# Optimization experiments

Measured on AMD Instinct MI355X. Metric: run time of the kernel, lower is better.

## Reference

```python
import jax, jax.numpy as jnp
import numpy as np

D_MODEL = 192
NODE_NUM = 64
DEPTH = 2
ALPHA = 0.05
NUM_LAYERS = 2
LN_EPS = 1e-5


def _gcn(x, p):
    # x: [N, in_dim*D_MODEL]; faithful port of GCN.forward (eval mode)
    nv1, nv2, ws, bs, wm, bm, we, be, wl, bl, g, b = p
    N = x.shape[0]
    in_dim = x.shape[1] // D_MODEL
    adp = jax.nn.softmax(jax.nn.relu(nv1 @ nv2), axis=1)            # [V,V]
    adj = adp + jnp.eye(NODE_NUM, dtype=x.dtype)
    a = adj / adj.sum(1, keepdims=True)                              # row-normalized
    h0 = jax.lax.conv_general_dilated(
        x.reshape(N, in_dim, D_MODEL), ws, (1,), 'VALID',
        dimension_numbers=('NCH', 'OIH', 'NCH')) + bs[None, :, None]  # [N,C,V]
    h = h0
    outs = [h0]
    for _ in range(DEPTH):
        h = ALPHA * h0 + (1.0 - ALPHA) * jnp.einsum('ncw,vw->ncv', h, a)
        outs.append(h)
    ho = jnp.concatenate(outs, axis=1)                               # [N,(DEPTH+1)C,V]
    ho = jax.nn.gelu(jnp.einsum('ncv,oc->nov', ho, wm) + bm[None, :, None], approximate=False)
    ho = jnp.einsum('ncv,oc->nov', ho, we) + be[None, :, None]       # [N,6,V]
    ho = jnp.einsum('nov,dv->nod', ho, wl) + bl                      # [N,6,D]
    mu = ho.mean(-1, keepdims=True)
    var = ((ho - mu) ** 2).mean(-1, keepdims=True)                   # biased, like torch LN
    ho = (ho - mu) / jnp.sqrt(var + LN_EPS) * g + b
    return ho.reshape(N, 6 * D_MODEL)


def _encoder(inp4, flag, layer_params):
    x = jnp.transpose(inp4, (2, 0, 1, 3)) if flag == 1 else jnp.transpose(inp4, (1, 0, 2, 3))
    W, B, O, D = x.shape
    L = W + O - 1
    N = W * B
    # input_transfer: shift row r by r along the slice axis
    place = jax.vmap(lambda xr, r: jax.lax.dynamic_update_slice(
        jnp.zeros((B, L, D), x.dtype), xr, (0, r, 0)))
    a = place(x, jnp.arange(W)).reshape(N, L, D)
    layer0_output = None
    output_all = None
    rows_layers, cols_layers = [], []
    for layer in range(NUM_LAYERS):
        if layer >= 1:
            a = output_all  # eval mode: F.dropout is identity
            if layer == 1:
                layer0_output = a
        p = layer_params[layer]

        def step(carry, x_t, p=p):
            h_row, h_col = carry
            gate = _gcn(jnp.concatenate([h_row, h_col, x_t], axis=-1), p)  # [N,6D]
            sg = jax.nn.sigmoid(gate[:, :4 * D])
            tg = jnp.tanh(gate[:, 4 * D:])
            ug_r, og_r, ug_c, og_c = jnp.split(sg, 4, axis=-1)
            ig_r, ig_c = jnp.split(tg, 2, axis=-1)
            h_row = jnp.tanh((1.0 - ug_r) * h_row + ug_r * ig_r) * og_r
            h_col = jnp.tanh((1.0 - ug_c) * h_col + ug_c * ig_c) * og_c
            out_s = jnp.concatenate([h_row, h_col], axis=-1)
            # col hidden is saved pre-roll, rolled for next step
            return (h_row, jnp.roll(h_col, B, axis=0)), (out_s, h_row, h_col)

        init = (jnp.zeros((N, D), x.dtype), jnp.zeros((N, D), x.dtype))
        _, (outs, hrows, hcols) = jax.lax.scan(step, init, jnp.swapaxes(a, 0, 1))
        output_all = jnp.swapaxes(outs, 0, 1)                        # [N,L,2D]
        if layer >= 1:
            output_all = output_all + layer0_output
        # rows saved at slice s>=O-1 from block loc = s-O+1
        rows = hrows.reshape(L, W, B, D)[jnp.arange(O - 1, L), jnp.arange(W)]  # [W,B,D]
        # cols saved at slice s>=W-1 from last batch block
        cols = hcols[W - 1:, (W - 1) * B:, :]                        # [O,B,D]
        rows_layers.append(rows)
        cols_layers.append(cols)
    hidden_row_all = jnp.stack(rows_layers).transpose(2, 0, 1, 3)    # [B,layers,W,D]
    hidden_col_all = jnp.stack(cols_layers).transpose(2, 0, 1, 3)    # [B,layers,O,D]
    if flag == 1:
        return output_all, hidden_col_all, hidden_row_all
    return output_all, hidden_row_all, hidden_col_all


def setup_inputs() -> dict:
    key = jax.random.key(0)
    ks = jax.random.split(key, 20)
    idx = [0]
    def nxt():
        k = ks[idx[0]]
        idx[0] += 1
        return k
    B, W, O = 8, 24, 48
    K = D_MODEL - NODE_NUM + 1  # 129
    cc, sc, nd = 16, 32, 40
    d = {"input": jax.random.normal(nxt(), (B, W, O, D_MODEL), dtype=jnp.float32)}
    for li, in_dim in enumerate([3, 4]):
        d[f"nodevec1_{li}"] = jax.random.normal(nxt(), (NODE_NUM, nd), dtype=jnp.float32)
        d[f"nodevec2_{li}"] = jax.random.normal(nxt(), (nd, NODE_NUM), dtype=jnp.float32)
        d[f"w_start_{li}"] = jax.random.normal(nxt(), (cc, in_dim, K), dtype=jnp.float32) * 0.05
        d[f"b_start_{li}"] = jnp.zeros((cc,), jnp.float32)
        d[f"w_mlp_{li}"] = jax.random.normal(nxt(), (sc, (DEPTH + 1) * cc), dtype=jnp.float32) * 0.05
        d[f"b_mlp_{li}"] = jnp.zeros((sc,), jnp.float32)
        d[f"w_end_{li}"] = jax.random.normal(nxt(), (6, sc), dtype=jnp.float32) * 0.05
        d[f"b_end_{li}"] = jnp.zeros((6,), jnp.float32)
        d[f"w_lin_{li}"] = jax.random.normal(nxt(), (D_MODEL, NODE_NUM), dtype=jnp.float32) * 0.05
        d[f"b_lin_{li}"] = jnp.zeros((D_MODEL,), jnp.float32)
        d[f"gamma_{li}"] = jnp.ones((D_MODEL,), jnp.float32)
        d[f"beta_{li}"] = jnp.zeros((D_MODEL,), jnp.float32)
    d["flag"] = 0
    return d


def reference(input, nodevec1_0, nodevec2_0, w_start_0, b_start_0, w_mlp_0, b_mlp_0,
              w_end_0, b_end_0, w_lin_0, b_lin_0, gamma_0, beta_0,
              nodevec1_1, nodevec2_1, w_start_1, b_start_1, w_mlp_1, b_mlp_1,
              w_end_1, b_end_1, w_lin_1, b_lin_1, gamma_1, beta_1, flag):
    p0 = (nodevec1_0, nodevec2_0, w_start_0, b_start_0, w_mlp_0, b_mlp_0,
          w_end_0, b_end_0, w_lin_0, b_lin_0, gamma_0, beta_0)
    p1 = (nodevec1_1, nodevec2_1, w_start_1, b_start_1, w_mlp_1, b_mlp_1,
          w_end_1, b_end_1, w_lin_1, b_lin_1, gamma_1, beta_1)
    return _encoder(input, flag, (p0, p1))
```

## Files before the change

### kernel.cpp

```cpp
#include <hip/hip_runtime.h>
#include <hip/hip_bf16.h>

#define NT 256
typedef unsigned short u16;

__device__ __forceinline__ u16 tobf(float x) {
  union { __hip_bfloat16 h; u16 u; } cv;
  cv.h = __float2bfloat16(x);
  return cv.u;
}
__device__ __forceinline__ float frombf(u16 u) {
  return __uint_as_float(((unsigned)u) << 16);
}
__device__ __forceinline__ float sigf(float x) {
  return __builtin_amdgcn_rcpf(1.f + __builtin_amdgcn_exp2f(-1.4426950408889634f * x));
}
__device__ __forceinline__ float tanh_fast(float x) {
  return 1.f - 2.f * __builtin_amdgcn_rcpf(1.f + __builtin_amdgcn_exp2f(2.8853900817779268f * x));
}

struct SeqArgs {
  const float* input;
  const float* nv1_0; const float* nv2_0; const float* nv1_1; const float* nv2_1;
  const float* w_start0; const float* b_start0; const float* w_mlp0; const float* b_mlp0;
  const float* w_end0;   const float* b_end0;   const float* w_lin0; const float* b_lin0;
  const float* gamma0;   const float* beta0;
  const float* w_start1; const float* b_start1; const float* w_mlp1; const float* b_mlp1;
  const float* w_end1;   const float* b_end1;   const float* w_lin1; const float* b_lin1;
  const float* gamma1;   const float* beta1;
  float* HCOL;
  int*   flags;
  float* out_all; float* out_hrow; float* out_hcol;
};

__global__ __launch_bounds__(NT, 1) void seq_kernel(SeqArgs A) {
  const int n = blockIdx.x, w = n >> 3, b = n & 7, tid = threadIdx.x;
  const int pred = (n + 184) % 192;

  __shared__ __align__(16) float sCIN[768];
  __shared__ __align__(16) u16   sWS[64 * 132];
  __shared__ __align__(16) float sAT[4096];
  __shared__ __align__(16) float sH[2][1024];
  __shared__ __align__(16) float sAbuf[4928];
  float* const sPart = sAbuf;
  float* const sG    = sAbuf;
  float* const sE    = sAbuf + 2048;
  float* const sY    = sAbuf;
  float* const smWE  = sAbuf + 3072;
  float* const smBE  = sAbuf + 3264;
  float* const smWM  = sAbuf + 3328;

  for (int layer = 0; layer < 2; ++layer) {
    const int in_dim = 3 + layer;
    const int P = in_dim - 1;
    const float* nv1    = layer ? A.nv1_1    : A.nv1_0;
    const float* nv2    = layer ? A.nv2_1    : A.nv2_0;
    const float* wstart = layer ? A.w_start1 : A.w_start0;
    const float* bs     = layer ? A.b_start1 : A.b_start0;
    const float* wm     = layer ? A.w_mlp1   : A.w_mlp0;
    const float* bm     = layer ? A.b_mlp1   : A.b_mlp0;
    const float* we     = layer ? A.w_end1   : A.w_end0;
    const float* be     = layer ? A.b_end1   : A.b_end0;
    const float* wl     = layer ? A.w_lin1   : A.w_lin0;
    const float* bl     = layer ? A.b_lin1   : A.b_lin0;
    const float* gm     = layer ? A.gamma1   : A.gamma0;
    const float* bt     = layer ? A.beta1    : A.beta0;

    for (int idx = tid; idx < 4096; idx += NT) {
      int v = idx >> 6, ww = idx & 63;
      float s = 0.f;
      for (int j = 0; j < 40; ++j) s = fmaf(nv1[v*40 + j], nv2[j*64 + ww], s);
      sAbuf[idx] = fmaxf(s, 0.f);
    }
    __syncthreads();
    if (tid < 64) {
      const int v = tid;
      float m = -1e30f;
      for (int ww = 0; ww < 64; ++ww) m = fmaxf(m, sAbuf[v*64 + ww]);
      float s = 0.f;
      for (int ww = 0; ww < 64; ++ww) { float e = expf(sAbuf[v*64 + ww] - m); sAbuf[v*64 + ww] = e; s += e; }
      float inv = 1.f / s, rs = 1.f;
      for (int ww = 0; ww < 64; ++ww) rs += sAbuf[v*64 + ww] * inv;
      float irs = 1.f / rs;
      for (int ww = 0; ww < 64; ++ww) {
        float a = sAbuf[v*64 + ww] * inv + ((ww == v) ? 1.f : 0.f);
        sAT[ww*64 + v] = a * irs;
      }
    }
    __syncthreads();
    for (int idx = tid; idx < 16*in_dim*132; idx += NT) {
      int row = idx / 132, k = idx - row*132;
      sWS[idx] = (k < 129) ? tobf(wstart[((row & 15)*in_dim + (row >> 4))*129 + k]) : (u16)0;
    }
    for (int idx = tid; idx < 1536; idx += NT) { int o = idx/48, c = idx - o*48; smWM[o*50 + c] = wm[idx]; }
    for (int idx = tid; idx < 192; idx += NT) smWE[idx] = we[idx];
    if (tid < 6) smBE[tid] = be[tid];
    for (int d = tid; d < 384; d += NT) sCIN[d] = 0.f;

    const int o_m = tid >> 3, v8 = (tid & 7)*8;
    const int v_p = tid & 63, cq = tid >> 6;
    const float bmv = bm[o_m];
    float blv = 0.f, gmv = 1.f, btv = 0.f;
    if (tid < 192) { blv = bl[tid]; gmv = gm[tid]; btv = bt[tid]; }
    float bs_r[4];
#pragma unroll
    for (int m = 0; m < 4; ++m) bs_r[m] = bs[(tid >> 6) + 4*m];
    __syncthreads();

    auto pre_phase = [&](int t) {
      if (layer == 0) {
        int o = t - w;
        if (o >= 0 && o < 48) {
          const float* xr = A.input + (((size_t)(b*24 + w)*48 + o)*192);
          for (int d = tid; d < 192; d += NT) sCIN[384 + d] = xr[d];
        } else {
          for (int d = tid; d < 192; d += NT) sCIN[384 + d] = 0.f;
        }
      } else {
        const float* xr = A.out_all + ((size_t)n*71 + t)*384;
        for (int d = tid; d < 384; d += NT) sCIN[384 + d] = xr[d];
      }
      __syncthreads();
      {
        const int ci = tid >> 2, vq = tid & 3;
        const int p = ci >> 4, c = ci & 15;
        if (p < P) {
          const int ich = (p == 0) ? 0 : (p + 1);
          float acc[16];
#pragma unroll
          for (int j = 0; j < 16; ++j) acc[j] = 0.f;
          const float* xin = (p == 0) ? &sCIN[vq*16] : &sCIN[384 + (p-1)*192 + vq*16];
          const u16* wrow = &sWS[(ich*16 + c)*132];
          for (int k4 = 0; k4 < 128; k4 += 4) {
            ushort4 wu = *(const ushort4*)(wrow + k4);
            float w0 = frombf(wu.x), w1 = frombf(wu.y), w2 = frombf(wu.z), w3 = frombf(wu.w);
            union { float4 v4[5]; float f[20]; } X;
#pragma unroll
            for (int m = 0; m < 5; ++m) X.v4[m] = *(const float4*)(xin + k4 + 4*m);
#pragma unroll
            for (int j = 0; j < 16; ++j) {
              acc[j] = fmaf(w0, X.f[j],   acc[j]);
              acc[j] = fmaf(w1, X.f[j+1], acc[j]);
              acc[j] = fmaf(w2, X.f[j+2], acc[j]);
              acc[j] = fmaf(w3, X.f[j+3], acc[j]);
            }
          }
          {
            float wk = frombf(wrow[128]);
            union { float4 v4[4]; float f[16]; } X;
#pragma unroll
            for (int m = 0; m < 4; ++m) X.v4[m] = *(const float4*)(xin + 128 + 4*m);
#pragma unroll
            for (int j = 0; j < 16; ++j) acc[j] = fmaf(wk, X.f[j], acc[j]);
          }
          float* pp = &sPart[(p*16 + c)*64 + vq*16];
#pragma unroll
          for (int m = 0; m < 4; ++m)
            *(float4*)(pp + 4*m) = make_float4(acc[4*m], acc[4*m+1], acc[4*m+2], acc[4*m+3]);
        }
      }
      __syncthreads();
      {
        int m = 0;
        for (int idx = tid; idx < 1024; idx += NT, ++m) {
          int c = idx >> 6, v = idx & 63;
          float s = bs_r[m];
          for (int p = 0; p < P; ++p) s += sPart[(p*16 + c)*64 + v];
          sH[0][idx] = s;
        }
      }
      __syncthreads();
    };
    pre_phase(0);

    for (int t = 0; t < 71; ++t) {
      const int S = layer*71 + t;

      if (t > 0) {
        if (tid == 0) {
          while (__hip_atomic_load(&A.flags[pred*32], __ATOMIC_ACQUIRE, __HIP_MEMORY_SCOPE_AGENT) < S)
            __builtin_amdgcn_s_sleep(1);
        }
        __syncthreads();
        float* hc = A.HCOL + ((size_t)((S-1) & 31)*192 + pred)*192;
        for (int d = tid; d < 192; d += NT)
          sCIN[192 + d] = __hip_atomic_load(&hc[d], __ATOMIC_RELAXED, __HIP_MEMORY_SCOPE_AGENT);
        __syncthreads();
      }

      {
        const int c = tid >> 4, vg = tid & 15;
        const float* xin = &sCIN[192 + vg*4];
        const u16* wrow = &sWS[(16 + c)*132];
        float4 a4 = *(const float4*)&sH[0][c*64 + vg*4];
        float a0 = a4.x, a1 = a4.y, a2 = a4.z, a3 = a4.w;
        float4 xc = *(const float4*)xin;
        for (int k4 = 0; k4 < 128; k4 += 4) {
          ushort4 wu = *(const ushort4*)(wrow + k4);
          float w0 = frombf(wu.x), w1 = frombf(wu.y), w2 = frombf(wu.z), w3 = frombf(wu.w);
          float4 xn = *(const float4*)(xin + k4 + 4);
          a0 = fmaf(w3, xc.w, fmaf(w2, xc.z, fmaf(w1, xc.y, fmaf(w0, xc.x, a0))));
          a1 = fmaf(w3, xn.x, fmaf(w2, xc.w, fmaf(w1, xc.z, fmaf(w0, xc.y, a1))));
          a2 = fmaf(w3, xn.y, fmaf(w2, xn.x, fmaf(w1, xc.w, fmaf(w0, xc.z, a2))));
          a3 = fmaf(w3, xn.z, fmaf(w2, xn.y, fmaf(w1, xn.x, fmaf(w0, xc.w, a3))));
          xc = xn;
        }
        float wk = frombf(wrow[128]);
        a0 = fmaf(wk, xc.x, a0); a1 = fmaf(wk, xc.y, a1);
        a2 = fmaf(wk, xc.z, a2); a3 = fmaf(wk, xc.w, a3);
        *(float4*)&sH[0][c*64 + vg*4] = make_float4(a0, a1, a2, a3);
      }
      __syncthreads();

      float g[8];
      {
#pragma unroll
        for (int j = 0; j < 8; ++j) g[j] = bmv;
        float pa[4] = {0.f, 0.f, 0.f, 0.f};
        for (int w4 = 0; w4 < 64; w4 += 4) {
          float a0 = sAT[(w4+0)*64 + v_p];
          float a1 = sAT[(w4+1)*64 + v_p];
          float a2 = sAT[(w4+2)*64 + v_p];
          float a3 = sAT[(w4+3)*64 + v_p];
#pragma unroll
          for (int j = 0; j < 4; ++j) {
            float4 h = *(const float4*)&sH[0][(cq*4 + j)*64 + w4];
            pa[j] = fmaf(h.x, a0, pa[j]); pa[j] = fmaf(h.y, a1, pa[j]);
            pa[j] = fmaf(h.z, a2, pa[j]); pa[j] = fmaf(h.w, a3, pa[j]);
          }
        }
#pragma unroll
        for (int j = 0; j < 4; ++j) {
          int c = cq*4 + j;
          sH[1][c*64 + v_p] = fmaf(0.95f, pa[j], 0.05f*sH[0][c*64 + v_p]);
        }
        for (int c = 0; c < 16; ++c) {
          float wv = smWM[o_m*50 + c];
          float4 ha = *(const float4*)&sH[0][c*64 + v8];
          float4 hb = *(const float4*)&sH[0][c*64 + v8 + 4];
          g[0]=fmaf(wv,ha.x,g[0]); g[1]=fmaf(wv,ha.y,g[1]); g[2]=fmaf(wv,ha.z,g[2]); g[3]=fmaf(wv,ha.w,g[3]);
          g[4]=fmaf(wv,hb.x,g[4]); g[5]=fmaf(wv,hb.y,g[5]); g[6]=fmaf(wv,hb.z,g[6]); g[7]=fmaf(wv,hb.w,g[7]);
        }
      }
      __syncthreads();

      {
        float pa[4] = {0.f, 0.f, 0.f, 0.f};
        for (int w4 = 0; w4 < 64; w4 += 4) {
          float a0 = sAT[(w4+0)*64 + v_p];
          float a1 = sAT[(w4+1)*64 + v_p];
          float a2 = sAT[(w4+2)*64 + v_p];
          float a3 = sAT[(w4+3)*64 + v_p];
#pragma unroll
          for (int j = 0; j < 4; ++j) {
            float4 h = *(const float4*)&sH[1][(cq*4 + j)*64 + w4];
            pa[j] = fmaf(h.x, a0, pa[j]); pa[j] = fmaf(h.y, a1, pa[j]);
            pa[j] = fmaf(h.z, a2, pa[j]); pa[j] = fmaf(h.w, a3, pa[j]);
          }
        }
#pragma unroll
        for (int j = 0; j < 4; ++j) {
          int c = cq*4 + j;
          float h0v = sH[0][c*64 + v_p];
          sH[0][c*64 + v_p] = fmaf(0.95f, pa[j], 0.05f*h0v);
        }
        for (int c = 0; c < 16; ++c) {
          float wv = smWM[o_m*50 + 16 + c];
          float4 ha = *(const float4*)&sH[1][c*64 + v8];
          float4 hb = *(const float4*)&sH[1][c*64 + v8 + 4];
          g[0]=fmaf(wv,ha.x,g[0]); g[1]=fmaf(wv,ha.y,g[1]); g[2]=fmaf(wv,ha.z,g[2]); g[3]=fmaf(wv,ha.w,g[3]);
          g[4]=fmaf(wv,hb.x,g[4]); g[5]=fmaf(wv,hb.y,g[5]); g[6]=fmaf(wv,hb.z,g[6]); g[7]=fmaf(wv,hb.w,g[7]);
        }
      }
      __syncthreads();

      {
        for (int c = 0; c < 16; ++c) {
          float wv = smWM[o_m*50 + 32 + c];
          float4 ha = *(const float4*)&sH[0][c*64 + v8];
          float4 hb = *(const float4*)&sH[0][c*64 + v8 + 4];
          g[0]=fmaf(wv,ha.x,g[0]); g[1]=fmaf(wv,ha.y,g[1]); g[2]=fmaf(wv,ha.z,g[2]); g[3]=fmaf(wv,ha.w,g[3]);
          g[4]=fmaf(wv,hb.x,g[4]); g[5]=fmaf(wv,hb.y,g[5]); g[6]=fmaf(wv,hb.z,g[6]); g[7]=fmaf(wv,hb.w,g[7]);
        }
#pragma unroll
        for (int j = 0; j < 8; ++j) {
          float x = g[j];
          g[j] = 0.5f * x * (1.f + erff(x * 0.70710678118654752f));
        }
        *(float4*)&sG[o_m*64 + v8]     = make_float4(g[0], g[1], g[2], g[3]);
        *(float4*)&sG[o_m*64 + v8 + 4] = make_float4(g[4], g[5], g[6], g[7]);
      }
      __syncthreads();

      for (int idx = tid; idx < 384; idx += NT) {
        int o2 = idx >> 6, v = idx & 63;
        float acc = smBE[o2];
        for (int c = 0; c < 32; ++c) acc = fmaf(smWE[o2*32 + c], sG[c*64 + v], acc);
        sE[idx] = acc;
      }
      __syncthreads();

      if (tid < 192) {
        const int d = tid;
        const float4* wrow = (const float4*)(wl + d*64);
        float y0=blv, y1=blv, y2=blv, y3=blv, y4=blv, y5=blv;
        for (int q = 0; q < 16; ++q) {
          float4 wv = wrow[q];
          float4 e0 = *(const float4*)&sE[0*64 + q*4];
          float4 e1 = *(const float4*)&sE[1*64 + q*4];
          float4 e2 = *(const float4*)&sE[2*64 + q*4];
          float4 e3 = *(const float4*)&sE[3*64 + q*4];
          float4 e4 = *(const float4*)&sE[4*64 + q*4];
          float4 e5 = *(const float4*)&sE[5*64 + q*4];
          y0 = fmaf(e0.x,wv.x, fmaf(e0.y,wv.y, fmaf(e0.z,wv.z, fmaf(e0.w,wv.w, y0))));
          y1 = fmaf(e1.x,wv.x, fmaf(e1.y,wv.y, fmaf(e1.z,wv.z, fmaf(e1.w,wv.w, y1))));
          y2 = fmaf(e2.x,wv.x, fmaf(e2.y,wv.y, fmaf(e2.z,wv.z, fmaf(e2.w,wv.w, y2))));
          y3 = fmaf(e3.x,wv.x, fmaf(e3.y,wv.y, fmaf(e3.z,wv.z, fmaf(e3.w,wv.w, y3))));
          y4 = fmaf(e4.x,wv.x, fmaf(e4.y,wv.y, fmaf(e4.z,wv.z, fmaf(e4.w,wv.w, y4))));
          y5 = fmaf(e5.x,wv.x, fmaf(e5.y,wv.y, fmaf(e5.z,wv.z, fmaf(e5.w,wv.w, y5))));
        }
        sY[0*192+d]=y0; sY[1*192+d]=y1; sY[2*192+d]=y2;
        sY[3*192+d]=y3; sY[4*192+d]=y4; sY[5*192+d]=y5;
      }
      __syncthreads();

      if (tid < 192) {
        const int r = tid >> 5, l32 = tid & 31;
        float sm = 0.f, sq = 0.f;
#pragma unroll
        for (int m = 0; m < 6; ++m) {
          float v = sY[r*192 + l32 + 32*m];
          sm += v; sq = fmaf(v, v, sq);
        }
#pragma unroll
        for (int off = 16; off >= 1; off >>= 1) {
          sm += __shfl_xor(sm, off);
          sq += __shfl_xor(sq, off);
        }
        if (l32 == 0) {
          float mu = sm * (1.f/192.f);
          float var = sq * (1.f/192.f) - mu*mu;
          sH[1][r] = mu;
          sH[1][8 + r] = rsqrtf(fmaxf(var, 0.f) + 1e-5f);
        }
      }
      __syncthreads();

      float hcn = 0.f;
      if (tid < 192) {
        const int d = tid;
        float y2 = fmaf((sY[2*192+d] - sH[1][2]) * sH[1][10], gmv, btv);
        float y3 = fmaf((sY[3*192+d] - sH[1][3]) * sH[1][11], gmv, btv);
        float y5 = fmaf((sY[5*192+d] - sH[1][5]) * sH[1][13], gmv, btv);
        float ugc = sigf(y2), ogc = sigf(y3), igc = tanh_fast(y5);
        float hc = sCIN[192 + d];
        hcn = tanh_fast(fmaf(ugc, igc, (1.f - ugc)*hc)) * ogc;
        __hip_atomic_store(&A.HCOL[((size_t)(S & 31)*192 + n)*192 + d], hcn,
                           __ATOMIC_RELAXED, __HIP_MEMORY_SCOPE_AGENT);
      }
      __syncthreads();
      if (tid == 0) {
        __threadfence();
        __hip_atomic_store(&A.flags[n*32], S + 1, __ATOMIC_RELEASE, __HIP_MEMORY_SCOPE_AGENT);
      }
      if (tid < 192) {
        const int d = tid;
        float y0 = fmaf((sY[0*192+d] - sH[1][0]) * sH[1][8],  gmv, btv);
        float y1 = fmaf((sY[1*192+d] - sH[1][1]) * sH[1][9],  gmv, btv);
        float y4 = fmaf((sY[4*192+d] - sH[1][4]) * sH[1][12], gmv, btv);
        float ugr = sigf(y0), ogr = sigf(y1), igr = tanh_fast(y4);
        float hr = sCIN[d];
        float hrn = tanh_fast(fmaf(ugr, igr, (1.f - ugr)*hr)) * ogr;
        sCIN[d] = hrn;
        float* oa = A.out_all + ((size_t)n*71 + t)*384;
        if (layer == 0) { oa[d] = hrn; oa[192 + d] = hcn; }
        else           { oa[d] = hrn + sCIN[384 + d]; oa[192 + d] = hcn + sCIN[576 + d]; }
        if (t == 47 + w)
          A.out_hrow[(((size_t)b*2 + layer)*24 + w)*192 + d] = hrn;
        if (w == 23 && t >= 23)
          A.out_hcol[(((size_t)b*2 + layer)*48 + (t - 23))*192 + d] = hcn;
      }
      __syncthreads();
      if (t < 70) pre_phase(t + 1);
    }
    __syncthreads();
  }
}

extern "C" void kernel_launch(void* const* d_in, const int* in_sizes, int n_in,
                              void* d_out, int out_size, void* d_ws, size_t ws_size,
                              hipStream_t stream) {
  (void)in_sizes; (void)n_in; (void)out_size; (void)ws_size;
  char* ws = (char*)d_ws;
  int*   flags = (int*)ws;
  float* HCOL  = (float*)(ws + 24576);

  hipMemsetAsync(flags, 0, 24576, stream);

  SeqArgs A;
  A.input    = (const float*)d_in[0];
  A.nv1_0    = (const float*)d_in[1];  A.nv2_0 = (const float*)d_in[2];
  A.w_start0 = (const float*)d_in[3];  A.b_start0 = (const float*)d_in[4];
  A.w_mlp0   = (const float*)d_in[5];  A.b_mlp0   = (const float*)d_in[6];
  A.w_end0   = (const float*)d_in[7];  A.b_end0   = (const float*)d_in[8];
  A.w_lin0   = (const float*)d_in[9];  A.b_lin0   = (const float*)d_in[10];
  A.gamma0   = (const float*)d_in[11]; A.beta0    = (const float*)d_in[12];
  A.nv1_1    = (const float*)d_in[13]; A.nv2_1 = (const float*)d_in[14];
  A.w_start1 = (const float*)d_in[15]; A.b_start1 = (const float*)d_in[16];
  A.w_mlp1   = (const float*)d_in[17]; A.b_mlp1   = (const float*)d_in[18];
  A.w_end1   = (const float*)d_in[19]; A.b_end1   = (const float*)d_in[20];
  A.w_lin1   = (const float*)d_in[21]; A.b_lin1   = (const float*)d_in[22];
  A.gamma1   = (const float*)d_in[23]; A.beta1    = (const float*)d_in[24];
  A.HCOL = HCOL; A.flags = flags;
  A.out_all  = (float*)d_out;
  A.out_hrow = (float*)d_out + 5234688;
  A.out_hcol = (float*)d_out + 5308416;

  seq_kernel<<<192, NT, 0, stream>>>(A);
}
```

Measured before the change: 2.872 ms.

## Double block size to 512 threads and redistribute per-step work across threads

Raises the thread count per block from 256 to 512 and remaps every stage of the sequential recurrence so each thread does less serial work. The start-conv now keeps per-thread register accumulators and no longer needs the partial-sum buffer and reduction pass. The linear/LayerNorm stage uses 384 threads and the row and column gate updates run concurrently on separate thread ranges. The aim is a shorter per-step critical path in this latency-bound recurrence, at the cost of more threads waiting at each barrier and some register-pressure risk.

```diff
diff --git a/kernel.cpp b/kernel.cpp
--- a/kernel.cpp
+++ b/kernel.cpp
@@ -1,7 +1,7 @@
 #include <hip/hip_runtime.h>
 #include <hip/hip_bf16.h>
 
-#define NT 256
+#define NT 512
 typedef unsigned short u16;
 
 __device__ __forceinline__ u16 tobf(float x) {
@@ -42,13 +42,20 @@
   __shared__ __align__(16) float sAT[4096];
   __shared__ __align__(16) float sH[2][1024];
   __shared__ __align__(16) float sAbuf[4928];
-  float* const sPart = sAbuf;
-  float* const sG    = sAbuf;
-  float* const sE    = sAbuf + 2048;
-  float* const sY    = sAbuf;
-  float* const smWE  = sAbuf + 3072;
-  float* const smBE  = sAbuf + 3264;
-  float* const smWM  = sAbuf + 3328;
+  float* const sG   = sAbuf;
+  float* const sY   = sAbuf;
+  float* const sE   = sAbuf + 2048;
+  float* const smWE = sAbuf + 3072;
+  float* const smBE = sAbuf + 3264;
+  float* const smWM = sAbuf + 3328;
+
+  const int c_cv = tid >> 5;
+  const int vj   = (tid & 31) * 2;
+  const int v_p  = tid & 63, cq2 = (tid >> 6) * 2;
+  const int o_m  = tid >> 4, v4 = (tid & 15) * 4;
+  const int dY   = (tid < 384) ? (tid - ((tid >= 192) ? 192 : 0)) : 0;
+  const int half = (tid >= 192);
+  const int dRC  = (tid < 192) ? tid : ((tid >= 256 && tid < 448) ? tid - 256 : -1);
 
   for (int layer = 0; layer < 2; ++layer) {
     const int in_dim = 3 + layer;
@@ -97,81 +104,55 @@
     if (tid < 6) smBE[tid] = be[tid];
     for (int d = tid; d < 384; d += NT) sCIN[d] = 0.f;
 
-    const int o_m = tid >> 3, v8 = (tid & 7)*8;
-    const int v_p = tid & 63, cq = tid >> 6;
     const float bmv = bm[o_m];
+    const float bs_c = bs[c_cv];
     float blv = 0.f, gmv = 1.f, btv = 0.f;
-    if (tid < 192) { blv = bl[tid]; gmv = gm[tid]; btv = bt[tid]; }
-    float bs_r[4];
-#pragma unroll
-    for (int m = 0; m < 4; ++m) bs_r[m] = bs[(tid >> 6) + 4*m];
-    __syncthreads();
-
-    auto pre_phase = [&](int t) {
+    if (tid < 384) blv = bl[dY];
+    if (dRC >= 0) { gmv = gm[dRC]; btv = bt[dRC]; }
+    __syncthreads();
+
+    auto stage_x = [&](int t) {
       if (layer == 0) {
         int o = t - w;
         if (o >= 0 && o < 48) {
-          const float* xr = A.input + (((size_t)(b*24 + w)*48 + o)*192);
-          for (int d = tid; d < 192; d += NT) sCIN[384 + d] = xr[d];
+          const float4* xr = (const float4*)(A.input + (((size_t)(b*24 + w)*48 + o)*192));
+          for (int i4 = tid; i4 < 48; i4 += NT) *(float4*)&sCIN[384 + i4*4] = xr[i4];
         } else {
           for (int d = tid; d < 192; d += NT) sCIN[384 + d] = 0.f;
         }
       } else {
-        const float* xr = A.out_all + ((size_t)n*71 + t)*384;
-        for (int d = tid; d < 384; d += NT) sCIN[384 + d] = xr[d];
-      }
-      __syncthreads();
-      {
-        const int ci = tid >> 2, vq = tid & 3;
-        const int p = ci >> 4, c = ci & 15;
-        if (p < P) {
-          const int ich = (p == 0) ? 0 : (p + 1);
-          float acc[16];
-#pragma unroll
-          for (int j = 0; j < 16; ++j) acc[j] = 0.f;
-          const float* xin = (p == 0) ? &sCIN[vq*16] : &sCIN[384 + (p-1)*192 + vq*16];
-          const u16* wrow = &sWS[(ich*16 + c)*132];
-          for (int k4 = 0; k4 < 128; k4 += 4) {
-            ushort4 wu = *(const ushort4*)(wrow + k4);
-            float w0 = frombf(wu.x), w1 = frombf(wu.y), w2 = frombf(wu.z), w3 = frombf(wu.w);
-            union { float4 v4[5]; float f[20]; } X;
-#pragma unroll
-            for (int m = 0; m < 5; ++m) X.v4[m] = *(const float4*)(xin + k4 + 4*m);
-#pragma unroll
-            for (int j = 0; j < 16; ++j) {
-              acc[j] = fmaf(w0, X.f[j],   acc[j]);
-              acc[j] = fmaf(w1, X.f[j+1], acc[j]);
-              acc[j] = fmaf(w2, X.f[j+2], acc[j]);
-              acc[j] = fmaf(w3, X.f[j+3], acc[j]);
-            }
-          }
-          {
-            float wk = frombf(wrow[128]);
-            union { float4 v4[4]; float f[16]; } X;
-#pragma unroll
-            for (int m = 0; m < 4; ++m) X.v4[m] = *(const float4*)(xin + 128 + 4*m);
-#pragma unroll
-            for (int j = 0; j < 16; ++j) acc[j] = fmaf(wk, X.f[j], acc[j]);
-          }
-          float* pp = &sPart[(p*16 + c)*64 + vq*16];
-#pragma unroll
-          for (int m = 0; m < 4; ++m)
-            *(float4*)(pp + 4*m) = make_float4(acc[4*m], acc[4*m+1], acc[4*m+2], acc[4*m+3]);
-        }
-      }
-      __syncthreads();
-      {
-        int m = 0;
-        for (int idx = tid; idx < 1024; idx += NT, ++m) {
-          int c = idx >> 6, v = idx & 63;
-          float s = bs_r[m];
-          for (int p = 0; p < P; ++p) s += sPart[(p*16 + c)*64 + v];
-          sH[0][idx] = s;
-        }
-      }
-      __syncthreads();
+        const float4* xr = (const float4*)(A.out_all + ((size_t)n*71 + t)*384);
+        for (int i4 = tid; i4 < 96; i4 += NT) *(float4*)&sCIN[384 + i4*4] = xr[i4];
+      }
     };
-    pre_phase(0);
+
+    float acc0, acc1;
+    auto conv_pre = [&]() {
+      float a0 = bs_c, a1 = bs_c;
+      for (int p = 0; p < P; ++p) {
+        const int ich = (p == 0) ? 0 : (p + 1);
+        const float* xin = (p == 0) ? &sCIN[vj] : &sCIN[384 + (p-1)*192 + vj];
+        const u16* wrow = &sWS[(ich*16 + c_cv)*132];
+        float2 c0 = *(const float2*)xin;
+        for (int k4 = 0; k4 < 128; k4 += 4) {
+          ushort4 wu = *(const ushort4*)(wrow + k4);
+          float w0 = frombf(wu.x), w1 = frombf(wu.y), w2 = frombf(wu.z), w3 = frombf(wu.w);
+          float2 c1 = *(const float2*)(xin + k4 + 2);
+          float2 n0 = *(const float2*)(xin + k4 + 4);
+          a0 = fmaf(w0,c0.x, fmaf(w1,c0.y, fmaf(w2,c1.x, fmaf(w3,c1.y, a0))));
+          a1 = fmaf(w0,c0.y, fmaf(w1,c1.x, fmaf(w2,c1.y, fmaf(w3,n0.x, a1))));
+          c0 = n0;
+        }
+        float wk = frombf(wrow[128]);
+        a0 = fmaf(wk, c0.x, a0);
+        a1 = fmaf(wk, c0.y, a1);
+      }
+      acc0 = a0; acc1 = a1;
+    };
+
+    stage_x(0);
+    __syncthreads();
+    conv_pre();
 
     for (int t = 0; t < 71; ++t) {
       const int S = layer*71 + t;
@@ -186,90 +167,74 @@
         for (int d = tid; d < 192; d += NT)
           sCIN[192 + d] = __hip_atomic_load(&hc[d], __ATOMIC_RELAXED, __HIP_MEMORY_SCOPE_AGENT);
         __syncthreads();
-      }
-
+
+        {
+          const float* xin = &sCIN[192 + vj];
+          const u16* wrow = &sWS[(16 + c_cv)*132];
+          float a0 = acc0, a1 = acc1;
+          float2 c0 = *(const float2*)xin;
+          for (int k4 = 0; k4 < 128; k4 += 4) {
+            ushort4 wu = *(const ushort4*)(wrow + k4);
+            float w0 = frombf(wu.x), w1 = frombf(wu.y), w2 = frombf(wu.z), w3 = frombf(wu.w);
+            float2 c1 = *(const float2*)(xin + k4 + 2);
+            float2 n0 = *(const float2*)(xin + k4 + 4);
+            a0 = fmaf(w0,c0.x, fmaf(w1,c0.y, fmaf(w2,c1.x, fmaf(w3,c1.y, a0))));
+            a1 = fmaf(w0,c0.y, fmaf(w1,c1.x, fmaf(w2,c1.y, fmaf(w3,n0.x, a1))));
+            c0 = n0;
+          }
+          float wk = frombf(wrow[128]);
+          a0 = fmaf(wk, c0.x, a0);
+          a1 = fmaf(wk, c0.y, a1);
+          *(float2*)&sH[0][c_cv*64 + vj] = make_float2(a0, a1);
+        }
+      } else {
+        *(float2*)&sH[0][c_cv*64 + vj] = make_float2(acc0, acc1);
+      }
+      __syncthreads();
+
+      float g[4];
       {
-        const int c = tid >> 4, vg = tid & 15;
-        const float* xin = &sCIN[192 + vg*4];
-        const u16* wrow = &sWS[(16 + c)*132];
-        float4 a4 = *(const float4*)&sH[0][c*64 + vg*4];
-        float a0 = a4.x, a1 = a4.y, a2 = a4.z, a3 = a4.w;
-        float4 xc = *(const float4*)xin;
-        for (int k4 = 0; k4 < 128; k4 += 4) {
-          ushort4 wu = *(const ushort4*)(wrow + k4);
-          float w0 = frombf(wu.x), w1 = frombf(wu.y), w2 = frombf(wu.z), w3 = frombf(wu.w);
-          float4 xn = *(const float4*)(xin + k4 + 4);
-          a0 = fmaf(w3, xc.w, fmaf(w2, xc.z, fmaf(w1, xc.y, fmaf(w0, xc.x, a0))));
-          a1 = fmaf(w3, xn.x, fmaf(w2, xc.w, fmaf(w1, xc.z, fmaf(w0, xc.y, a1))));
-          a2 = fmaf(w3, xn.y, fmaf(w2, xn.x, fmaf(w1, xc.w, fmaf(w0, xc.z, a2))));
-          a3 = fmaf(w3, xn.z, fmaf(w2, xn.y, fmaf(w1, xn.x, fmaf(w0, xc.w, a3))));
-          xc = xn;
-        }
-        float wk = frombf(wrow[128]);
-        a0 = fmaf(wk, xc.x, a0); a1 = fmaf(wk, xc.y, a1);
-        a2 = fmaf(wk, xc.z, a2); a3 = fmaf(wk, xc.w, a3);
-        *(float4*)&sH[0][c*64 + vg*4] = make_float4(a0, a1, a2, a3);
-      }
-      __syncthreads();
-
-      float g[8];
-      {
-#pragma unroll
-        for (int j = 0; j < 8; ++j) g[j] = bmv;
-        float pa[4] = {0.f, 0.f, 0.f, 0.f};
+        g[0] = bmv; g[1] = bmv; g[2] = bmv; g[3] = bmv;
+        float pa0 = 0.f, pa1 = 0.f;
         for (int w4 = 0; w4 < 64; w4 += 4) {
           float a0 = sAT[(w4+0)*64 + v_p];
           float a1 = sAT[(w4+1)*64 + v_p];
           float a2 = sAT[(w4+2)*64 + v_p];
           float a3 = sAT[(w4+3)*64 + v_p];
-#pragma unroll
-          for (int j = 0; j < 4; ++j) {
-            float4 h = *(const float4*)&sH[0][(cq*4 + j)*64 + w4];
-            pa[j] = fmaf(h.x, a0, pa[j]); pa[j] = fmaf(h.y, a1, pa[j]);
-            pa[j] = fmaf(h.z, a2, pa[j]); pa[j] = fmaf(h.w, a3, pa[j]);
-          }
-        }
-#pragma unroll
-        for (int j = 0; j < 4; ++j) {
-          int c = cq*4 + j;
-          sH[1][c*64 + v_p] = fmaf(0.95f, pa[j], 0.05f*sH[0][c*64 + v_p]);
-        }
+          float4 h0 = *(const float4*)&sH[0][cq2*64 + w4];
+          float4 h1 = *(const float4*)&sH[0][(cq2+1)*64 + w4];
+          pa0 = fmaf(h0.x,a0, fmaf(h0.y,a1, fmaf(h0.z,a2, fmaf(h0.w,a3, pa0))));
+          pa1 = fmaf(h1.x,a0, fmaf(h1.y,a1, fmaf(h1.z,a2, fmaf(h1.w,a3, pa1))));
+        }
+        sH[1][cq2*64 + v_p]     = fmaf(0.95f, pa0, 0.05f*sH[0][cq2*64 + v_p]);
+        sH[1][(cq2+1)*64 + v_p] = fmaf(0.95f, pa1, 0.05f*sH[0][(cq2+1)*64 + v_p]);
         for (int c = 0; c < 16; ++c) {
           float wv = smWM[o_m*50 + c];
-          float4 ha = *(const float4*)&sH[0][c*64 + v8];
-          float4 hb = *(const float4*)&sH[0][c*64 + v8 + 4];
-          g[0]=fmaf(wv,ha.x,g[0]); g[1]=fmaf(wv,ha.y,g[1]); g[2]=fmaf(wv,ha.z,g[2]); g[3]=fmaf(wv,ha.w,g[3]);
-          g[4]=fmaf(wv,hb.x,g[4]); g[5]=fmaf(wv,hb.y,g[5]); g[6]=fmaf(wv,hb.z,g[6]); g[7]=fmaf(wv,hb.w,g[7]);
+          float4 hh = *(const float4*)&sH[0][c*64 + v4];
+          g[0]=fmaf(wv,hh.x,g[0]); g[1]=fmaf(wv,hh.y,g[1]); g[2]=fmaf(wv,hh.z,g[2]); g[3]=fmaf(wv,hh.w,g[3]);
         }
       }
       __syncthreads();
 
       {
-        float pa[4] = {0.f, 0.f, 0.f, 0.f};
+        float pa0 = 0.f, pa1 = 0.f;
         for (int w4 = 0; w4 < 64; w4 += 4) {
           float a0 = sAT[(w4+0)*64 + v_p];
           float a1 = sAT[(w4+1)*64 + v_p];
           float a2 = sAT[(w4+2)*64 + v_p];
           float a3 = sAT[(w4+3)*64 + v_p];
-#pragma unroll
-          for (int j = 0; j < 4; ++j) {
-            float4 h = *(const float4*)&sH[1][(cq*4 + j)*64 + w4];
-            pa[j] = fmaf(h.x, a0, pa[j]); pa[j] = fmaf(h.y, a1, pa[j]);
-            pa[j] = fmaf(h.z, a2, pa[j]); pa[j] = fmaf(h.w, a3, pa[j]);
-          }
-        }
-#pragma unroll
-        for (int j = 0; j < 4; ++j) {
-          int c = cq*4 + j;
-          float h0v = sH[0][c*64 + v_p];
-          sH[0][c*64 + v_p] = fmaf(0.95f, pa[j], 0.05f*h0v);
-        }
+          float4 h0 = *(const float4*)&sH[1][cq2*64 + w4];
+          float4 h1 = *(const float4*)&sH[1][(cq2+1)*64 + w4];
+          pa0 = fmaf(h0.x,a0, fmaf(h0.y,a1, fmaf(h0.z,a2, fmaf(h0.w,a3, pa0))));
+          pa1 = fmaf(h1.x,a0, fmaf(h1.y,a1, fmaf(h1.z,a2, fmaf(h1.w,a3, pa1))));
+        }
+        float h00 = sH[0][cq2*64 + v_p], h01 = sH[0][(cq2+1)*64 + v_p];
+        sH[0][cq2*64 + v_p]     = fmaf(0.95f, pa0, 0.05f*h00);
+        sH[0][(cq2+1)*64 + v_p] = fmaf(0.95f, pa1, 0.05f*h01);
         for (int c = 0; c < 16; ++c) {
           float wv = smWM[o_m*50 + 16 + c];
-          float4 ha = *(const float4*)&sH[1][c*64 + v8];
-          float4 hb = *(const float4*)&sH[1][c*64 + v8 + 4];
-          g[0]=fmaf(wv,ha.x,g[0]); g[1]=fmaf(wv,ha.y,g[1]); g[2]=fmaf(wv,ha.z,g[2]); g[3]=fmaf(wv,ha.w,g[3]);
-          g[4]=fmaf(wv,hb.x,g[4]); g[5]=fmaf(wv,hb.y,g[5]); g[6]=fmaf(wv,hb.z,g[6]); g[7]=fmaf(wv,hb.w,g[7]);
+          float4 hh = *(const float4*)&sH[1][c*64 + v4];
+          g[0]=fmaf(wv,hh.x,g[0]); g[1]=fmaf(wv,hh.y,g[1]); g[2]=fmaf(wv,hh.z,g[2]); g[3]=fmaf(wv,hh.w,g[3]);
         }
       }
       __syncthreads();
@@ -277,67 +242,59 @@
       {
         for (int c = 0; c < 16; ++c) {
           float wv = smWM[o_m*50 + 32 + c];
-          float4 ha = *(const float4*)&sH[0][c*64 + v8];
-          float4 hb = *(const float4*)&sH[0][c*64 + v8 + 4];
-          g[0]=fmaf(wv,ha.x,g[0]); g[1]=fmaf(wv,ha.y,g[1]); g[2]=fmaf(wv,ha.z,g[2]); g[3]=fmaf(wv,ha.w,g[3]);
-          g[4]=fmaf(wv,hb.x,g[4]); g[5]=fmaf(wv,hb.y,g[5]); g[6]=fmaf(wv,hb.z,g[6]); g[7]=fmaf(wv,hb.w,g[7]);
+          float4 hh = *(const float4*)&sH[0][c*64 + v4];
+          g[0]=fmaf(wv,hh.x,g[0]); g[1]=fmaf(wv,hh.y,g[1]); g[2]=fmaf(wv,hh.z,g[2]); g[3]=fmaf(wv,hh.w,g[3]);
         }
 #pragma unroll
-        for (int j = 0; j < 8; ++j) {
+        for (int j = 0; j < 4; ++j) {
           float x = g[j];
           g[j] = 0.5f * x * (1.f + erff(x * 0.70710678118654752f));
         }
-        *(float4*)&sG[o_m*64 + v8]     = make_float4(g[0], g[1], g[2], g[3]);
-        *(float4*)&sG[o_m*64 + v8 + 4] = make_float4(g[4], g[5], g[6], g[7]);
-      }
-      __syncthreads();
-
-      for (int idx = tid; idx < 384; idx += NT) {
-        int o2 = idx >> 6, v = idx & 63;
+        *(float4*)&sG[o_m*64 + v4] = make_float4(g[0], g[1], g[2], g[3]);
+      }
+      __syncthreads();
+
+      if (tid < 384) {
+        int o2 = tid >> 6, v = tid & 63;
         float acc = smBE[o2];
         for (int c = 0; c < 32; ++c) acc = fmaf(smWE[o2*32 + c], sG[c*64 + v], acc);
-        sE[idx] = acc;
-      }
-      __syncthreads();
-
-      if (tid < 192) {
-        const int d = tid;
-        const float4* wrow = (const float4*)(wl + d*64);
-        float y0=blv, y1=blv, y2=blv, y3=blv, y4=blv, y5=blv;
+        sE[tid] = acc;
+      }
+      __syncthreads();
+
+      if (tid < 384) {
+        const float4* wrow = (const float4*)(wl + dY*64);
+        const float* sEb = sE + half*192;
+        float y0 = blv, y1 = blv, y2 = blv;
         for (int q = 0; q < 16; ++q) {
           float4 wv = wrow[q];
-          float4 e0 = *(const float4*)&sE[0*64 + q*4];
-          float4 e1 = *(const float4*)&sE[1*64 + q*4];
-          float4 e2 = *(const float4*)&sE[2*64 + q*4];
-          float4 e3 = *(const float4*)&sE[3*64 + q*4];
-          float4 e4 = *(const float4*)&sE[4*64 + q*4];
-          float4 e5 = *(const float4*)&sE[5*64 + q*4];
+          float4 e0 = *(const float4*)&sEb[0*64 + q*4];
+          float4 e1 = *(const float4*)&sEb[1*64 + q*4];
+          float4 e2 = *(const float4*)&sEb[2*64 + q*4];
           y0 = fmaf(e0.x,wv.x, fmaf(e0.y,wv.y, fmaf(e0.z,wv.z, fmaf(e0.w,wv.w, y0))));
           y1 = fmaf(e1.x,wv.x, fmaf(e1.y,wv.y, fmaf(e1.z,wv.z, fmaf(e1.w,wv.w, y1))));
           y2 = fmaf(e2.x,wv.x, fmaf(e2.y,wv.y, fmaf(e2.z,wv.z, fmaf(e2.w,wv.w, y2))));
-          y3 = fmaf(e3.x,wv.x, fmaf(e3.y,wv.y, fmaf(e3.z,wv.z, fmaf(e3.w,wv.w, y3))));
-          y4 = fmaf(e4.x,wv.x, fmaf(e4.y,wv.y, fmaf(e4.z,wv.z, fmaf(e4.w,wv.w, y4))));
-          y5 = fmaf(e5.x,wv.x, fmaf(e5.y,wv.y, fmaf(e5.z,wv.z, fmaf(e5.w,wv.w, y5))));
-        }
-        sY[0*192+d]=y0; sY[1*192+d]=y1; sY[2*192+d]=y2;
-        sY[3*192+d]=y3; sY[4*192+d]=y4; sY[5*192+d]=y5;
-      }
-      __syncthreads();
-
-      if (tid < 192) {
-        const int r = tid >> 5, l32 = tid & 31;
+        }
+        sY[(half*3 + 0)*192 + dY] = y0;
+        sY[(half*3 + 1)*192 + dY] = y1;
+        sY[(half*3 + 2)*192 + dY] = y2;
+      }
+      __syncthreads();
+
+      if (tid < 384) {
+        int r = tid >> 6, l = tid & 63;
         float sm = 0.f, sq = 0.f;
 #pragma unroll
-        for (int m = 0; m < 6; ++m) {
-          float v = sY[r*192 + l32 + 32*m];
+        for (int m2 = 0; m2 < 3; ++m2) {
+          float v = sY[r*192 + l + 64*m2];
           sm += v; sq = fmaf(v, v, sq);
         }
 #pragma unroll
-        for (int off = 16; off >= 1; off >>= 1) {
+        for (int off = 32; off >= 1; off >>= 1) {
           sm += __shfl_xor(sm, off);
           sq += __shfl_xor(sq, off);
         }
-        if (l32 == 0) {
+        if (l == 0) {
           float mu = sm * (1.f/192.f);
           float var = sq * (1.f/192.f) - mu*mu;
           sH[1][r] = mu;
@@ -346,42 +303,51 @@
       }
       __syncthreads();
 
-      float hcn = 0.f;
+      float hrn = 0.f, rx0 = 0.f, rx1 = 0.f;
       if (tid < 192) {
         const int d = tid;
-        float y2 = fmaf((sY[2*192+d] - sH[1][2]) * sH[1][10], gmv, btv);
-        float y3 = fmaf((sY[3*192+d] - sH[1][3]) * sH[1][11], gmv, btv);
-        float y5 = fmaf((sY[5*192+d] - sH[1][5]) * sH[1][13], gmv, btv);
+        float y2 = fmaf((sY[384 + d] - sH[1][2]) * sH[1][10], gmv, btv);
+        float y3 = fmaf((sY[576 + d] - sH[1][3]) * sH[1][11], gmv, btv);
+        float y5 = fmaf((sY[960 + d] - sH[1][5]) * sH[1][13], gmv, btv);
         float ugc = sigf(y2), ogc = sigf(y3), igc = tanh_fast(y5);
         float hc = sCIN[192 + d];
-        hcn = tanh_fast(fmaf(ugc, igc, (1.f - ugc)*hc)) * ogc;
+        float hcn = tanh_fast(fmaf(ugc, igc, (1.f - ugc)*hc)) * ogc;
+        sH[1][32 + d] = hcn;
         __hip_atomic_store(&A.HCOL[((size_t)(S & 31)*192 + n)*192 + d], hcn,
                            __ATOMIC_RELAXED, __HIP_MEMORY_SCOPE_AGENT);
-      }
-      __syncthreads();
+      } else if (dRC >= 0) {
+        const int d = dRC;
+        float y0 = fmaf((sY[d]       - sH[1][0]) * sH[1][8],  gmv, btv);
+        float y1 = fmaf((sY[192 + d] - sH[1][1]) * sH[1][9],  gmv, btv);
+        float y4 = fmaf((sY[768 + d] - sH[1][4]) * sH[1][12], gmv, btv);
+        float ugr = sigf(y0), ogr = sigf(y1), igr = tanh_fast(y4);
+        float hr = sCIN[d];
+        hrn = tanh_fast(fmaf(ugr, igr, (1.f - ugr)*hr)) * ogr;
+        sCIN[d] = hrn;
+        if (layer) { rx0 = sCIN[384 + d]; rx1 = sCIN[576 + d]; }
+      }
+      __syncthreads();
+
       if (tid == 0) {
         __threadfence();
         __hip_atomic_store(&A.flags[n*32], S + 1, __ATOMIC_RELEASE, __HIP_MEMORY_SCOPE_AGENT);
       }
-      if (tid < 192) {
-        const int d = tid;
-        float y0 = fmaf((sY[0*192+d] - sH[1][0]) * sH[1][8],  gmv, btv);
-        float y1 = fmaf((sY[1*192+d] - sH[1][1]) * sH[1][9],  gmv, btv);
-        float y4 = fmaf((sY[4*192+d] - sH[1][4]) * sH[1][12], gmv, btv);
-        float ugr = sigf(y0), ogr = sigf(y1), igr = tanh_fast(y4);
-        float hr = sCIN[d];
-        float hrn = tanh_fast(fmaf(ugr, igr, (1.f - ugr)*hr)) * ogr;
-        sCIN[d] = hrn;
+      if (tid >= 256 && tid < 448) {
+        const int d = dRC;
+        float hcn = sH[1][32 + d];
         float* oa = A.out_all + ((size_t)n*71 + t)*384;
         if (layer == 0) { oa[d] = hrn; oa[192 + d] = hcn; }
-        else           { oa[d] = hrn + sCIN[384 + d]; oa[192 + d] = hcn + sCIN[576 + d]; }
+        else            { oa[d] = hrn + rx0; oa[192 + d] = hcn + rx1; }
         if (t == 47 + w)
           A.out_hrow[(((size_t)b*2 + layer)*24 + w)*192 + d] = hrn;
         if (w == 23 && t >= 23)
           A.out_hcol[(((size_t)b*2 + layer)*48 + (t - 23))*192 + d] = hcn;
       }
-      __syncthreads();
-      if (t < 70) pre_phase(t + 1);
+      if (t < 70) {
+        stage_x(t + 1);
+        __syncthreads();
+        conv_pre();
+      }
     }
     __syncthreads();
   }
```

New measurement: 10.49 ms. +265.2%, slower.
